# Optimization experiments

Hardware: AMD Instinct MI355X
Metric: run time of the kernel (lower is better)

## Reference

```python
import jax, jax.numpy as jnp
import numpy as np

V = 1024      # token vocab
C = 8         # n_codebooks
T = 256       # seg_len
BP = 4        # block_pairs (n_latent_blocks)
K = 512       # latent_vocab_size (codebook entries)
E = 128       # emb_dim
D = 128       # latent_dim / d_model
BETA = 0.05
NB = 6 * BP   # decoder sequence length = 24
NH = 4
HD = D // NH
FF = 512
R = 8
IN_FLAT = NB * D
OUT = T * C * V
B = 32


def setup_inputs() -> dict:
    key = jax.random.key(0)
    ks = jax.random.split(key, 20)
    n = lambda i, shape, s=0.02: jax.random.normal(ks[i], shape, jnp.float32) * s
    return {
        "tokens_prev": jax.random.randint(ks[0], (B, T, C), 0, V, jnp.int32),
        "tokens_curr": jax.random.randint(ks[1], (B, T, C), 0, V, jnp.int32),
        "tokens_next": jax.random.randint(ks[2], (B, T, C), 0, V, jnp.int32),
        "emb": n(3, (V, E)),
        "conv1_w": n(4, (4 * D, E * C, 3)),
        "conv1_b": jnp.zeros((4 * D,), jnp.float32),
        "conv2_w": n(5, (2 * D, 4 * D, 1)),
        "conv2_b": jnp.zeros((2 * D,), jnp.float32),
        "cb_instru": jax.random.uniform(ks[6], (K, D), jnp.float32, -1.0 / K, 1.0 / K),
        "cb_vocal": jax.random.uniform(ks[7], (K, D), jnp.float32, -1.0 / K, 1.0 / K),
        "pos": n(8, (1, NB, D), 1.0),
        "attn_in_w": n(9, (3 * D, D)),
        "attn_in_b": jnp.zeros((3 * D,), jnp.float32),
        "attn_out_w": n(10, (D, D)),
        "attn_out_b": jnp.zeros((D,), jnp.float32),
        "ln1_g": jnp.ones((D,), jnp.float32),
        "ln1_b": jnp.zeros((D,), jnp.float32),
        "lin1_w": n(11, (FF, D)),
        "lin1_b": jnp.zeros((FF,), jnp.float32),
        "lin2_w": n(12, (D, FF)),
        "lin2_b": jnp.zeros((D,), jnp.float32),
        "ln2_g": jnp.ones((D,), jnp.float32),
        "ln2_b": jnp.zeros((D,), jnp.float32),
        "lora_a": n(13, (R, IN_FLAT), 0.01),
        "lora_b": n(14, (OUT, R), 0.01),
    }


def _conv1d(x, w, b, pad):
    # x: (B, Cin, L), w: (Cout, Cin, Kw)
    y = jax.lax.conv_general_dilated(x, w, window_strides=(1,), padding=[(pad, pad)],
                                     dimension_numbers=("NCH", "OIH", "NCH"))
    return y + b[None, :, None]


def _encode(tokens, emb, w1, b1, w2, b2):
    Bb, Tt, Cc = tokens.shape
    x = emb[tokens].reshape(Bb, Tt, -1).transpose(0, 2, 1)       # (B, C*E, T)
    x = jax.nn.relu(_conv1d(x, w1, b1, 1))                        # (B, 4D, T)
    x = jax.nn.relu(_conv1d(x, w2, b2, 0))                        # (B, 2D, T)
    # AdaptiveAvgPool1d(BP) with T % BP == 0 -> mean over contiguous chunks
    x = x.reshape(Bb, 2 * D, BP, Tt // BP).mean(-1).transpose(0, 2, 1)  # (B, BP, 2D)
    return x[..., :D], x[..., D:]


def _vq(z, codebook):
    # z: (B, N, D); eval-mode VQ (no EMA update)
    Bb, N, Dd = z.shape
    flat = z.reshape(-1, Dd)
    dist = (jnp.sum(flat * flat, axis=1, keepdims=True)
            - 2.0 * flat @ codebook.T
            + jnp.sum(codebook * codebook, axis=1))
    codes = jnp.argmin(dist, axis=1)
    z_q = codebook[codes].reshape(Bb, N, Dd)
    commit = jnp.mean((z - jax.lax.stop_gradient(z_q)) ** 2)
    loss = BETA * commit
    z_q_st = z + jax.lax.stop_gradient(z_q - z)
    return z_q_st, codes.reshape(Bb, N), loss


def _layer_norm(x, g, b):
    mu = x.mean(-1, keepdims=True)
    var = ((x - mu) ** 2).mean(-1, keepdims=True)
    return (x - mu) * jax.lax.rsqrt(var + 1e-5) * g + b


def _tf_layer(x, in_w, in_b, out_w, out_b, g1, b1, w1, bb1, w2, bb2, g2, b2):
    # Post-norm TransformerEncoderLayer (relu, eval/no-dropout). x: (B, S, D)
    Bb, S, Dd = x.shape
    qkv = x @ in_w.T + in_b
    q, k, v = jnp.split(qkv, 3, axis=-1)
    q = q.reshape(Bb, S, NH, HD).transpose(0, 2, 1, 3)
    k = k.reshape(Bb, S, NH, HD).transpose(0, 2, 1, 3)
    v = v.reshape(Bb, S, NH, HD).transpose(0, 2, 1, 3)
    attn = jax.nn.softmax(jnp.einsum("bhsd,bhtd->bhst", q, k) / np.sqrt(HD), axis=-1)
    o = jnp.einsum("bhst,bhtd->bhsd", attn, v).transpose(0, 2, 1, 3).reshape(Bb, S, Dd)
    x = _layer_norm(x + o @ out_w.T + out_b, g1, b1)
    ff = jax.nn.relu(x @ w1.T + bb1) @ w2.T + bb2
    return _layer_norm(x + ff, g2, b2)


def reference(tokens_prev, tokens_curr, tokens_next, emb, conv1_w, conv1_b,
              conv2_w, conv2_b, cb_instru, cb_vocal, pos, attn_in_w, attn_in_b,
              attn_out_w, attn_out_b, ln1_g, ln1_b, lin1_w, lin1_b, lin2_w,
              lin2_b, ln2_g, ln2_b, lora_a, lora_b):
    p_i, p_v = _encode(tokens_prev, emb, conv1_w, conv1_b, conv2_w, conv2_b)
    c_i, c_v = _encode(tokens_curr, emb, conv1_w, conv1_b, conv2_w, conv2_b)
    n_i, n_v = _encode(tokens_next, emb, conv1_w, conv1_b, conv2_w, conv2_b)
    p_i_q, _, l1 = _vq(p_i, cb_instru)
    c_i_q, _, l2 = _vq(c_i, cb_instru)
    n_i_q, _, l3 = _vq(n_i, cb_instru)
    p_v_q, _, l4 = _vq(p_v, cb_vocal)
    c_v_q, _, l5 = _vq(c_v, cb_vocal)
    n_v_q, _, l6 = _vq(n_v, cb_vocal)
    vq_loss = l1 + l2 + l3 + l4 + l5 + l6
    z = jnp.concatenate([p_i_q, p_v_q, c_i_q, c_v_q, n_i_q, n_v_q], axis=1)  # (B, 24, D)
    z = z + pos[:, :z.shape[1], :]
    z = _tf_layer(z, attn_in_w, attn_in_b, attn_out_w, attn_out_b,
                  ln1_g, ln1_b, lin1_w, lin1_b, lin2_w, lin2_b, ln2_g, ln2_b)
    Bb = z.shape[0]
    flat = z.reshape(Bb, -1)
    logits = (flat @ lora_a.T) @ lora_b.T          # (B, T*C*V)
    logits = logits.reshape(Bb, T, C, V)
    logp = jax.nn.log_softmax(logits, axis=-1)
    nll = -jnp.take_along_axis(logp, tokens_curr[..., None].astype(jnp.int32), axis=-1)
    recon_loss = nll.mean()
    total_loss = recon_loss + vq_loss
    return total_loss
```

## Files before the change

kernel.cpp:

```cpp
#include <hip/hip_runtime.h>
#include <hip/hip_bf16.h>
#include <cstdint>
#include <cstddef>

typedef __attribute__((ext_vector_type(8))) short short8;
typedef __attribute__((ext_vector_type(4))) float floatx4;


__device__ __forceinline__ ushort f2bf(float f) {
    union { float f; unsigned int u; } x; x.f = f;
    unsigned int r = (x.u + 0x7fffu + ((x.u >> 16) & 1u)) >> 16;
    return (ushort)r;
}
__device__ __forceinline__ float bf2f(ushort u) {
    union { unsigned int u; float f; } x; x.u = ((unsigned int)u) << 16;
    return x.f;
}

__global__ __launch_bounds__(256) void prep_all(
    const float* __restrict__ emb, const float* __restrict__ w1,
    const float* __restrict__ w2, const float* __restrict__ cbi,
    const float* __restrict__ cbv, const float* __restrict__ aiw,
    const float* __restrict__ aow, const float* __restrict__ l1w,
    const float* __restrict__ l2w,
    ushort* __restrict__ ebf, ushort* __restrict__ w1bf, ushort* __restrict__ w2bf,
    float* __restrict__ cbiT, float* __restrict__ cbvT,
    ushort* __restrict__ aiwbf, ushort* __restrict__ aowbf,
    ushort* __restrict__ l1wbf, ushort* __restrict__ l2wbf,
    float* __restrict__ accum)
{
    int idx = blockIdx.x * 256 + threadIdx.x;
    if (idx < 4) accum[idx] = 0.f;
    if (idx < 131072) {
        ebf[idx] = f2bf(emb[idx]);
    } else if (idx < 262144) {
        int j = idx - 131072; w2bf[j] = f2bf(w2[j]);
    } else if (idx < 327680) {
        int j = idx - 262144; cbiT[(j & 127) * 512 + (j >> 7)] = cbi[j];
    } else if (idx < 393216) {
        int j = idx - 327680; cbvT[(j & 127) * 512 + (j >> 7)] = cbv[j];
    } else if (idx < 442368) {
        int j = idx - 393216; aiwbf[j] = f2bf(aiw[j]);
    } else if (idx < 475136) {
        int j = idx - 442368; aowbf[j] = f2bf(aow[j]);
    } else if (idx < 540672) {
        int j = idx - 475136; l1wbf[j] = f2bf(l1w[j]);
    } else if (idx < 606208) {
        int j = idx - 540672; l2wbf[j] = f2bf(l2w[j]);
    } else if (idx < 2179072) {
        int j = idx - 606208;
        int e  = j & 127;
        int co = (j >> 7) & 511;
        int cc = (j >> 16) & 7;
        int kw = j >> 19;
        w1bf[j] = f2bf(w1[(co * 1024 + cc * 128 + e) * 3 + kw]);
    }
}

__global__ __launch_bounds__(512, 4) void conv1_mfma(
    const int* __restrict__ tp, const int* __restrict__ tcu, const int* __restrict__ tn,
    const ushort* __restrict__ ebf, const ushort* __restrict__ w1bf,
    const float* __restrict__ b1, ushort* __restrict__ y1)
{
    constexpr int LDA = 136;
    __shared__ ushort As[130 * LDA];
    __shared__ ushort Bs[128 * LDA];
    __shared__ int tokL[130 * 8];
    const int tid = threadIdx.x;
    const int bx = blockIdx.x;
    const int nb = bx & 3, mb = bx >> 2;
    const int set = mb >> 6, rem = mb & 63, bb = rem >> 1, t0 = (rem & 1) << 7;
    const int n0 = nb << 7;
    const int* tok = (set == 0) ? tp : ((set == 1) ? tcu : tn);

    for (int idx = tid; idx < 1040; idx += 512) {
        const int row = idx >> 3, cc = idx & 7;
        const int gt = t0 + row - 1;
        tokL[idx] = (gt >= 0 && gt < 256) ? tok[bb * 2048 + gt * 8 + cc] : -1;
    }

    const int w = tid >> 6, lane = tid & 63;
    const int wm = w & 1, wn = w >> 1;
    const int rA = lane & 15, q4 = lane >> 4;
    const int ch = tid & 15, rowst = tid >> 4;

    floatx4 acc[4][2];
    for (int mi = 0; mi < 4; ++mi)
        for (int ni = 0; ni < 2; ++ni)
            acc[mi][ni] = (floatx4)(0.0f);

    __syncthreads();

    for (int cc = 0; cc < 8; ++cc) {
        for (int p = 0; p < 5; ++p) {
            const int row = p * 32 + rowst;
            if (row < 130) {
                const int tk = tokL[row * 8 + cc];
                uint4 val = make_uint4(0u, 0u, 0u, 0u);
                if (tk >= 0) val = *(const uint4*)(ebf + tk * 128 + ch * 8);
                *(uint4*)(As + row * LDA + ch * 8) = val;
            }
        }
        for (int kw = 0; kw < 3; ++kw) {
            const ushort* wsrc = w1bf + ((size_t)((kw * 8 + cc) * 512 + n0)) * 128;
            for (int p = 0; p < 4; ++p) {
                const int row = p * 32 + rowst;
                *(uint4*)(Bs + row * LDA + ch * 8) = *(const uint4*)(wsrc + row * 128 + ch * 8);
            }
            __syncthreads();
            for (int ks = 0; ks < 4; ++ks) {
                const int k0 = ks * 32 + q4 * 8;
                short8 a[4], bfr[2];
                for (int mi = 0; mi < 4; ++mi)
                    a[mi] = *(const short8*)(As + (wm * 64 + mi * 16 + rA + kw) * LDA + k0);
                for (int ni = 0; ni < 2; ++ni)
                    bfr[ni] = *(const short8*)(Bs + (wn * 32 + ni * 16 + rA) * LDA + k0);
                for (int mi = 0; mi < 4; ++mi)
                    for (int ni = 0; ni < 2; ++ni)
                        acc[mi][ni] = __builtin_amdgcn_mfma_f32_16x16x32_bf16(
                            a[mi], bfr[ni], acc[mi][ni], 0, 0, 0);
            }
            __syncthreads();
        }
    }
    for (int ni = 0; ni < 2; ++ni) {
        const int co = n0 + wn * 32 + ni * 16 + rA;
        const float bias = b1[co];
        for (int mi = 0; mi < 4; ++mi) {
            for (int r = 0; r < 4; ++r) {
                const int t = t0 + wm * 64 + mi * 16 + q4 * 4 + r;
                float v = acc[mi][ni][r] + bias;
                v = v > 0.f ? v : 0.f;
                y1[((size_t)(set * 32 + bb) * 256 + t) * 512 + co] = f2bf(v);
            }
        }
    }
}

__global__ __launch_bounds__(512, 4) void conv2_mfma(
    const ushort* __restrict__ y1, const ushort* __restrict__ w2bf,
    const float* __restrict__ b2, float* __restrict__ y2)
{
    constexpr int LDA = 136;
    __shared__ ushort As[128 * LDA];
    __shared__ ushort Bs[128 * LDA];
    __shared__ float pool[256];
    const int tid = threadIdx.x;
    const int bx = blockIdx.x;
    const int nb = bx & 1, mb = bx >> 1;
    const int set = mb >> 6, rem = mb & 63, bb = rem >> 1, t0 = (rem & 1) << 7;
    const int n0 = nb << 7;
    const int w = tid >> 6, lane = tid & 63;
    const int wm = w & 1, wn = w >> 1;
    const int rA = lane & 15, q4 = lane >> 4;
    const int ch = tid & 15, rowst = tid >> 4;

    floatx4 acc[4][2];
    for (int mi = 0; mi < 4; ++mi)
        for (int ni = 0; ni < 2; ++ni)
            acc[mi][ni] = (floatx4)(0.0f);

    const size_t arowbase = ((size_t)(set * 32 + bb) * 256 + t0) * 512;
    for (int kc = 0; kc < 4; ++kc) {
        for (int p = 0; p < 4; ++p) {
            const int row = p * 32 + rowst;
            *(uint4*)(As + row * LDA + ch * 8) =
                *(const uint4*)(y1 + arowbase + (size_t)row * 512 + kc * 128 + ch * 8);
            *(uint4*)(Bs + row * LDA + ch * 8) =
                *(const uint4*)(w2bf + (size_t)(n0 + row) * 512 + kc * 128 + ch * 8);
        }
        __syncthreads();
        for (int ks = 0; ks < 4; ++ks) {
            const int k0 = ks * 32 + q4 * 8;
            short8 a[4], bfr[2];
            for (int mi = 0; mi < 4; ++mi)
                a[mi] = *(const short8*)(As + (wm * 64 + mi * 16 + rA) * LDA + k0);
            for (int ni = 0; ni < 2; ++ni)
                bfr[ni] = *(const short8*)(Bs + (wn * 32 + ni * 16 + rA) * LDA + k0);
            for (int mi = 0; mi < 4; ++mi)
                for (int ni = 0; ni < 2; ++ni)
                    acc[mi][ni] = __builtin_amdgcn_mfma_f32_16x16x32_bf16(
                        a[mi], bfr[ni], acc[mi][ni], 0, 0, 0);
        }
        __syncthreads();
    }
    for (int ni = 0; ni < 2; ++ni) {
        const int col = wn * 32 + ni * 16 + rA;
        const float bias = b2[n0 + col];
        float s = 0.f;
        for (int mi = 0; mi < 4; ++mi)
            for (int r = 0; r < 4; ++r) {
                float v = acc[mi][ni][r] + bias;
                s += v > 0.f ? v : 0.f;
            }
        s += __shfl_xor(s, 16);
        s += __shfl_xor(s, 32);
        if (q4 == 0) pool[wm * 128 + col] = s;
    }
    __syncthreads();
    if (tid < 256) {
        const int wrow = tid >> 7, col = tid & 127;
        const int p = (t0 >> 6) + wrow;
        y2[((size_t)(set * 32 + bb) * 4 + p) * 256 + n0 + col] = pool[tid] * (1.f / 64.f);
    }
}

__global__ __launch_bounds__(256) void vq_kernel(
    const float* __restrict__ y2, const float* __restrict__ cbiT, const float* __restrict__ cbvT,
    const float* __restrict__ cbi, const float* __restrict__ cbv,
    const float* __restrict__ pos, float* __restrict__ ztr, ushort* __restrict__ xbf,
    float* __restrict__ accum)
{
    const int q = blockIdx.x;
    const int tid = threadIdx.x;
    const int set = q >> 7, bb = (q >> 2) & 31, p = q & 3;
    __shared__ float zloc[256];
    __shared__ float bestv[4];
    __shared__ int   besti[4];
    __shared__ int   code_sh[2];
    __shared__ float wsum2[4];
    zloc[tid] = y2[(size_t)q * 256 + tid];
    __syncthreads();
    const int w = tid >> 6, lane = tid & 63;
    const int half = w >> 1, sub = w & 1;
    const float4* cbT4 = (const float4*)(half ? cbvT : cbiT);
    const float* zh = zloc + half * 128;
    const int k4 = sub * 64 + lane;
    float a0 = 0.f, a1 = 0.f, a2 = 0.f, a3 = 0.f;
    for (int d = 0; d < 128; ++d) {
        float4 v = cbT4[d * 128 + k4];
        const float z = zh[d];
        float d0 = z - v.x, d1 = z - v.y, d2 = z - v.z, d3 = z - v.w;
        a0 += d0 * d0; a1 += d1 * d1; a2 += d2 * d2; a3 += d3 * d3;
    }
    float best = a0; int bidx = k4 * 4;
    if (a1 < best) { best = a1; bidx = k4 * 4 + 1; }
    if (a2 < best) { best = a2; bidx = k4 * 4 + 2; }
    if (a3 < best) { best = a3; bidx = k4 * 4 + 3; }
    for (int off = 32; off > 0; off >>= 1) {
        float ov = __shfl_xor(best, off);
        int   oi = __shfl_xor(bidx, off);
        if (ov < best || (ov == best && oi < bidx)) { best = ov; bidx = oi; }
    }
    if (lane == 0) { bestv[w] = best; besti[w] = bidx; }
    __syncthreads();
    if (tid < 2) {
        float v0 = bestv[tid * 2], v1 = bestv[tid * 2 + 1];
        int   i0 = besti[tid * 2], i1 = besti[tid * 2 + 1];
        code_sh[tid] = (v1 < v0 || (v1 == v0 && i1 < i0)) ? i1 : i0;
    }
    __syncthreads();
    const int hh = tid >> 7, d = tid & 127;
    const int code = code_sh[hh];
    const float* cb = hh ? cbv : cbi;
    const float zq = cb[code * 128 + d];
    const float diff = zloc[hh * 128 + d] - zq;
    float sq = diff * diff;
    for (int off = 32; off > 0; off >>= 1) sq += __shfl_xor(sq, off);
    if (lane == 0) wsum2[w] = sq;
    const int s = (set * 2 + hh) * 4 + p;
    const float val = zq + pos[s * 128 + d];
    ztr[((size_t)bb * 24 + s) * 128 + d] = val;
    xbf[((size_t)bb * 24 + s) * 128 + d] = f2bf(val);
    __syncthreads();
    if (tid == 0) atomicAdd(&accum[0], wsum2[0] + wsum2[1] + wsum2[2] + wsum2[3]);
}

template<int KTOT, int NTOT, int RELU, int OUTBF>
__global__ __launch_bounds__(256) void gemm64_kernel(
    const ushort* __restrict__ A, const ushort* __restrict__ Bw,
    const float* __restrict__ bias, void* __restrict__ Co)
{
    constexpr int NBLK = NTOT / 64;
    constexpr int LDA = 136;
    __shared__ ushort As[64 * LDA];
    __shared__ ushort Bs[64 * LDA];
    const int tid = threadIdx.x;
    const int mblk = blockIdx.x / NBLK, nblk = blockIdx.x % NBLK;
    const int m0 = mblk * 64, n0 = nblk * 64;
    const int w = tid >> 6, lane = tid & 63;
    const int rA = lane & 15, q4 = lane >> 4;
    const int ch = tid & 15, rowst = tid >> 4;

    floatx4 acc[4];
    for (int mi = 0; mi < 4; ++mi) acc[mi] = (floatx4)(0.f);

    for (int kc = 0; kc < KTOT / 128; ++kc) {
        for (int i = 0; i < 4; ++i) {
            const int row = i * 16 + rowst;
            *(uint4*)(As + row * LDA + ch * 8) =
                *(const uint4*)(A + (size_t)(m0 + row) * KTOT + kc * 128 + ch * 8);
            *(uint4*)(Bs + row * LDA + ch * 8) =
                *(const uint4*)(Bw + (size_t)(n0 + row) * KTOT + kc * 128 + ch * 8);
        }
        __syncthreads();
        for (int ks = 0; ks < 4; ++ks) {
            const int k0 = ks * 32 + q4 * 8;
            short8 bfr = *(const short8*)(Bs + (w * 16 + rA) * LDA + k0);
            for (int mi = 0; mi < 4; ++mi) {
                short8 a = *(const short8*)(As + (mi * 16 + rA) * LDA + k0);
                acc[mi] = __builtin_amdgcn_mfma_f32_16x16x32_bf16(a, bfr, acc[mi], 0, 0, 0);
            }
        }
        __syncthreads();
    }
    const int col = n0 + w * 16 + rA;
    const float bs = bias[col];
    for (int mi = 0; mi < 4; ++mi) {
        for (int r = 0; r < 4; ++r) {
            const int row = m0 + mi * 16 + q4 * 4 + r;
            float vv = acc[mi][r] + bs;
            if (RELU) vv = vv > 0.f ? vv : 0.f;
            if (OUTBF) ((ushort*)Co)[(size_t)row * NTOT + col] = f2bf(vv);
            else       ((float*)Co)[(size_t)row * NTOT + col]  = vv;
        }
    }
}

template<int KTOT, int WRITE_F32>
__global__ __launch_bounds__(256) void gemm_ln_kernel(
    const ushort* __restrict__ A, const ushort* __restrict__ Bw,
    const float* __restrict__ bias, const float* __restrict__ resid,
    const float* __restrict__ g, const float* __restrict__ beta,
    ushort* __restrict__ outbf, float* __restrict__ outf)
{
    constexpr int LDA = 136;
    __shared__ ushort As[64 * LDA];
    __shared__ ushort Bs[128 * LDA];
    __shared__ float ps[64 * 4], pq[64 * 4], muv[64], invv[64];
    const int tid = threadIdx.x;
    const int m0 = blockIdx.x * 64;
    const int w = tid >> 6, lane = tid & 63;
    const int rA = lane & 15, q4 = lane >> 4;
    const int ch = tid & 15, rowst = tid >> 4;

    floatx4 acc[4][2];
    for (int mi = 0; mi < 4; ++mi)
        for (int ni = 0; ni < 2; ++ni)
            acc[mi][ni] = (floatx4)(0.f);

    for (int kc = 0; kc < KTOT / 128; ++kc) {
        for (int i = 0; i < 4; ++i) {
            const int row = i * 16 + rowst;
            *(uint4*)(As + row * LDA + ch * 8) =
                *(const uint4*)(A + (size_t)(m0 + row) * KTOT + kc * 128 + ch * 8);
        }
        for (int i = 0; i < 8; ++i) {
            const int row = i * 16 + rowst;
            *(uint4*)(Bs + row * LDA + ch * 8) =
                *(const uint4*)(Bw + (size_t)row * KTOT + kc * 128 + ch * 8);
        }
        __syncthreads();
        for (int ks = 0; ks < 4; ++ks) {
            const int k0 = ks * 32 + q4 * 8;
            short8 a[4], bfr[2];
            for (int mi = 0; mi < 4; ++mi)
                a[mi] = *(const short8*)(As + (mi * 16 + rA) * LDA + k0);
            for (int ni = 0; ni < 2; ++ni)
                bfr[ni] = *(const short8*)(Bs + ((w * 2 + ni) * 16 + rA) * LDA + k0);
            for (int mi = 0; mi < 4; ++mi)
                for (int ni = 0; ni < 2; ++ni)
                    acc[mi][ni] = __builtin_amdgcn_mfma_f32_16x16x32_bf16(
                        a[mi], bfr[ni], acc[mi][ni], 0, 0, 0);
        }
        __syncthreads();
    }
    for (int ni = 0; ni < 2; ++ni) {
        const int col = (w * 2 + ni) * 16 + rA;
        const float bs = bias[col];
        for (int mi = 0; mi < 4; ++mi)
            for (int r = 0; r < 4; ++r) {
                const int row = m0 + mi * 16 + q4 * 4 + r;
                acc[mi][ni][r] += bs + resid[(size_t)row * 128 + col];
            }
    }
    for (int mi = 0; mi < 4; ++mi)
        for (int r = 0; r < 4; ++r) {
            float s  = acc[mi][0][r] + acc[mi][1][r];
            float sq = acc[mi][0][r] * acc[mi][0][r] + acc[mi][1][r] * acc[mi][1][r];
            for (int off = 1; off < 16; off <<= 1) {
                s  += __shfl_xor(s, off);
                sq += __shfl_xor(sq, off);
            }
            if (rA == 0) {
                const int rl = mi * 16 + q4 * 4 + r;
                ps[rl * 4 + w] = s;
                pq[rl * 4 + w] = sq;
            }
        }
    __syncthreads();
    if (tid < 64) {
        float s  = ps[tid * 4] + ps[tid * 4 + 1] + ps[tid * 4 + 2] + ps[tid * 4 + 3];
        float sq = pq[tid * 4] + pq[tid * 4 + 1] + pq[tid * 4 + 2] + pq[tid * 4 + 3];
        float mu = s * (1.f / 128.f);
        float var = sq * (1.f / 128.f) - mu * mu;
        muv[tid] = mu;
        invv[tid] = rsqrtf(var + 1e-5f);
    }
    __syncthreads();
    for (int ni = 0; ni < 2; ++ni) {
        const int col = (w * 2 + ni) * 16 + rA;
        const float gg = g[col], bb = beta[col];
        for (int mi = 0; mi < 4; ++mi)
            for (int r = 0; r < 4; ++r) {
                const int rl = mi * 16 + q4 * 4 + r;
                const int row = m0 + rl;
                float v = (acc[mi][ni][r] - muv[rl]) * invv[rl] * gg + bb;
                outbf[(size_t)row * 128 + col] = f2bf(v);
                if (WRITE_F32) outf[(size_t)row * 128 + col] = v;
            }
    }
}

__global__ __launch_bounds__(64) void attn_kernel(
    const float* __restrict__ qkvb, ushort* __restrict__ obuf)
{
    const int bh = blockIdx.x;
    const int b = bh >> 2, h = bh & 3;
    const int tid = threadIdx.x;
    __shared__ float q[24 * 32], k[24 * 32], v[24 * 32], sc[24 * 24];
    for (int i = 0; i < 12; ++i) {
        const int idx = i * 64 + tid;
        const int s = idx >> 5, d = idx & 31;
        const size_t base = ((size_t)(b * 24 + s)) * 384 + h * 32 + d;
        q[idx] = qkvb[base];
        k[idx] = qkvb[base + 128];
        v[idx] = qkvb[base + 256];
    }
    __syncthreads();
    for (int i = 0; i < 9; ++i) {
        const int e = i * 64 + tid;
        const int si = e / 24, j = e - si * 24;
        float a = 0.f;
        for (int d = 0; d < 32; ++d) a += q[si * 32 + d] * k[j * 32 + d];
        sc[si * 24 + j] = a * 0.17677669529663687f;
    }
    __syncthreads();
    if (tid < 24) {
        float* row = sc + tid * 24;
        float m = row[0];
        for (int j = 1; j < 24; ++j) m = row[j] > m ? row[j] : m;
        float ssum = 0.f;
        for (int j = 0; j < 24; ++j) { float e = __expf(row[j] - m); row[j] = e; ssum += e; }
        float inv = 1.f / ssum;
        for (int j = 0; j < 24; ++j) row[j] *= inv;
    }
    __syncthreads();
    for (int i = 0; i < 12; ++i) {
        const int idx = i * 64 + tid;
        const int s = idx >> 5, d = idx & 31;
        float a = 0.f;
        for (int j = 0; j < 24; ++j) a += sc[s * 24 + j] * v[j * 32 + d];
        obuf[((size_t)(b * 24 + s)) * 128 + h * 32 + d] = f2bf(a);
    }
}

__global__ __launch_bounds__(256) void lora_kernel(
    const ushort* __restrict__ zbf, const float* __restrict__ lora_a,
    float* __restrict__ hbuf)
{
    const int b = blockIdx.x;
    const int tid = threadIdx.x;
    const int w = tid >> 6, lane = tid & 63;
    __shared__ float zl[3072];
    for (int idx = tid; idx < 3072; idx += 256) zl[idx] = bf2f(zbf[(size_t)b * 3072 + idx]);
    __syncthreads();
    for (int rr = 0; rr < 2; ++rr) {
        const int r = w + rr * 4;
        float acc = 0.f;
        for (int idx = lane; idx < 3072; idx += 64)
            acc += lora_a[(size_t)r * 3072 + idx] * zl[idx];
        for (int off = 32; off > 0; off >>= 1) acc += __shfl_xor(acc, off);
        if (lane == 0) hbuf[b * 8 + r] = acc;
    }
}

__global__ __launch_bounds__(256) void logits_kernel(
    const float* __restrict__ hbuf, const float* __restrict__ lora_b,
    const int* __restrict__ tokc, float* __restrict__ accum, float* __restrict__ out)
{
    const int tid = threadIdx.x;
    const int tcb = blockIdx.x;
    __shared__ float hl[256];
    __shared__ float wsum[4];
    __shared__ float ltok;
    hl[tid] = hbuf[tid];
    float wr[4][8];
    for (int i = 0; i < 4; ++i) {
        const float4* pw = (const float4*)(lora_b + ((size_t)tcb * 1024 + tid + 256 * i) * 8);
        float4 x = pw[0], y = pw[1];
        wr[i][0] = x.x; wr[i][1] = x.y; wr[i][2] = x.z; wr[i][3] = x.w;
        wr[i][4] = y.x; wr[i][5] = y.y; wr[i][6] = y.z; wr[i][7] = y.w;
    }
    __syncthreads();
    float nll = 0.f;
    for (int bb = 0; bb < 32; ++bb) {
        const int tv = tokc[bb * 2048 + tcb];
        const float* h = hl + bb * 8;
        float h0 = h[0], h1 = h[1], h2 = h[2], h3 = h[3];
        float h4 = h[4], h5 = h[5], h6 = h[6], h7 = h[7];
        float sl = 0.f;
        for (int i = 0; i < 4; ++i) {
            float lg = h0 * wr[i][0] + h1 * wr[i][1] + h2 * wr[i][2] + h3 * wr[i][3]
                     + h4 * wr[i][4] + h5 * wr[i][5] + h6 * wr[i][6] + h7 * wr[i][7];
            sl += __expf(lg);
            if (tid + 256 * i == tv) ltok = lg;
        }
        for (int off = 32; off > 0; off >>= 1) sl += __shfl_xor(sl, off);
        if ((tid & 63) == 0) wsum[tid >> 6] = sl;
        __syncthreads();
        if (tid == 0) nll += logf(wsum[0] + wsum[1] + wsum[2] + wsum[3]) - ltok;
        __syncthreads();
    }
    if (tid == 0) {
        atomicAdd(&accum[1], nll);
        __threadfence();
        unsigned int prev = atomicAdd((unsigned int*)(accum + 2), 1u);
        if (prev == 2047u) {
            float vq  = atomicAdd(&accum[0], 0.f);
            float rec = atomicAdd(&accum[1], 0.f);
            out[0] = rec * (1.f / 65536.f) + 0.05f * vq * (1.f / 16384.f);
        }
    }
}

extern "C" void kernel_launch(void* const* d_in, const int* in_sizes, int n_in,
                              void* d_out, int out_size, void* d_ws, size_t ws_size,
                              hipStream_t stream) {
    const int*   tp   = (const int*)d_in[0];
    const int*   tcu  = (const int*)d_in[1];
    const int*   tn   = (const int*)d_in[2];
    const float* emb  = (const float*)d_in[3];
    const float* w1   = (const float*)d_in[4];
    const float* b1   = (const float*)d_in[5];
    const float* w2   = (const float*)d_in[6];
    const float* b2   = (const float*)d_in[7];
    const float* cbi  = (const float*)d_in[8];
    const float* cbv  = (const float*)d_in[9];
    const float* pos  = (const float*)d_in[10];
    const float* aiw  = (const float*)d_in[11];
    const float* aib  = (const float*)d_in[12];
    const float* aow  = (const float*)d_in[13];
    const float* aob  = (const float*)d_in[14];
    const float* g1   = (const float*)d_in[15];
    const float* be1  = (const float*)d_in[16];
    const float* l1w  = (const float*)d_in[17];
    const float* l1b  = (const float*)d_in[18];
    const float* l2w  = (const float*)d_in[19];
    const float* l2b  = (const float*)d_in[20];
    const float* g2   = (const float*)d_in[21];
    const float* be2  = (const float*)d_in[22];
    const float* lra  = (const float*)d_in[23];
    const float* lrb  = (const float*)d_in[24];

    char* wsb = (char*)d_ws;
    ushort* ebf  = (ushort*)(wsb + 0);
    ushort* w1bf = (ushort*)(wsb + 262144);
    ushort* w2bf = (ushort*)(wsb + 3407872);
    float*  cbiT = (float*)(wsb + 3670016);
    float*  cbvT = (float*)(wsb + 3932160);
    ushort* y1   = (ushort*)(wsb + 4194304);
    float*  y2   = (float*)(wsb + 29360128);
    float*  ztr  = (float*)(wsb + 29753344);
    float*  hbuf = (float*)(wsb + 30146560);
    float*  accum= (float*)(wsb + 30147584);
    ushort* aiwbf= (ushort*)(wsb + 30147648);
    ushort* aowbf= (ushort*)(wsb + 30245952);
    ushort* l1wbf= (ushort*)(wsb + 30278720);
    ushort* l2wbf= (ushort*)(wsb + 30409792);
    if (ws_size < 30540864) return;

    float*  qkvb = (float*)(wsb + 4194304);
    ushort* obuf = (ushort*)(wsb + 5373952);
    ushort* x1bf = (ushort*)(wsb + 5570560);
    float*  x1f  = (float*)(wsb + 5767168);
    ushort* hff  = (ushort*)(wsb + 6160384);
    ushort* zbf  = (ushort*)(wsb + 6946816);
    ushort* xbf  = (ushort*)(wsb + 7143424);

    prep_all<<<8512, 256, 0, stream>>>(emb, w1, w2, cbi, cbv, aiw, aow, l1w, l2w,
                                       ebf, w1bf, w2bf, cbiT, cbvT,
                                       aiwbf, aowbf, l1wbf, l2wbf, accum);
    conv1_mfma<<<768, 512, 0, stream>>>(tp, tcu, tn, ebf, w1bf, b1, y1);
    conv2_mfma<<<384, 512, 0, stream>>>(y1, w2bf, b2, y2);
    vq_kernel<<<384, 256, 0, stream>>>(y2, cbiT, cbvT, cbi, cbv, pos, ztr, xbf, accum);
    gemm64_kernel<128, 384, 0, 0><<<72, 256, 0, stream>>>(xbf, aiwbf, aib, qkvb);
    attn_kernel<<<128, 64, 0, stream>>>(qkvb, obuf);
    gemm_ln_kernel<128, 1><<<12, 256, 0, stream>>>(obuf, aowbf, aob, ztr, g1, be1, x1bf, x1f);
    gemm64_kernel<128, 512, 1, 1><<<96, 256, 0, stream>>>(x1bf, l1wbf, l1b, hff);
    gemm_ln_kernel<512, 0><<<12, 256, 0, stream>>>(hff, l2wbf, l2b, x1f, g2, be2, zbf, nullptr);
    lora_kernel<<<32, 256, 0, stream>>>(zbf, lra, hbuf);
    logits_kernel<<<2048, 256, 0, stream>>>(hbuf, lrb, tcu, accum, (float*)d_out);
}
```

Baseline: 404.4 us.

## Precompute embedding-conv1 product table and fuse transformer tail into persistent kernel

```diff
diff --git a/kernel.cpp b/kernel.cpp
--- a/kernel.cpp
+++ b/kernel.cpp
@@ -15,6 +15,17 @@
 __device__ __forceinline__ float bf2f(ushort u) {
     union { unsigned int u; float f; } x; x.u = ((unsigned int)u) << 16;
     return x.f;
+}
+
+__device__ __forceinline__ void gbar(unsigned int* bar, unsigned int nb) {
+    __threadfence();
+    __syncthreads();
+    if (threadIdx.x == 0) {
+        atomicAdd(bar, 1u);
+        while (atomicAdd(bar, 0u) < nb) __builtin_amdgcn_s_sleep(2);
+    }
+    __syncthreads();
+    __threadfence();
 }
 
 __global__ __launch_bounds__(256) void prep_all(
@@ -30,7 +41,7 @@
     float* __restrict__ accum)
 {
     int idx = blockIdx.x * 256 + threadIdx.x;
-    if (idx < 4) accum[idx] = 0.f;
+    if (idx < 16) accum[idx] = 0.f;
     if (idx < 131072) {
         ebf[idx] = f2bf(emb[idx]);
     } else if (idx < 262144) {
@@ -57,6 +68,108 @@
     }
 }
 
+__global__ __launch_bounds__(512) void ubuild_kernel(
+    const ushort* __restrict__ ebf, const ushort* __restrict__ w1bf,
+    ushort* __restrict__ U)
+{
+    constexpr int LDA = 136;
+    __shared__ ushort As[128 * LDA];
+    __shared__ ushort Bs[128 * LDA];
+    const int tid = threadIdx.x;
+    const int bx = blockIdx.x;
+    const int kc = bx >> 5, rem = bx & 31, mt = rem >> 2, nt = rem & 3;
+    const int v0 = mt << 7, co0 = nt << 7;
+    const int w = tid >> 6, lane = tid & 63;
+    const int wm = w & 1, wn = w >> 1;
+    const int rA = lane & 15, q4 = lane >> 4;
+    const int ch = tid & 15, rowst = tid >> 4;
+
+    for (int p = 0; p < 4; ++p) {
+        const int row = p * 32 + rowst;
+        *(uint4*)(As + row * LDA + ch * 8) =
+            *(const uint4*)(ebf + (size_t)(v0 + row) * 128 + ch * 8);
+        *(uint4*)(Bs + row * LDA + ch * 8) =
+            *(const uint4*)(w1bf + (size_t)kc * 65536 + (size_t)(co0 + row) * 128 + ch * 8);
+    }
+    __syncthreads();
+
+    floatx4 acc[4][2];
+    for (int mi = 0; mi < 4; ++mi)
+        for (int ni = 0; ni < 2; ++ni)
+            acc[mi][ni] = (floatx4)(0.0f);
+    for (int ks = 0; ks < 4; ++ks) {
+        const int k0 = ks * 32 + q4 * 8;
+        short8 a[4], bfr[2];
+        for (int mi = 0; mi < 4; ++mi)
+            a[mi] = *(const short8*)(As + (wm * 64 + mi * 16 + rA) * LDA + k0);
+        for (int ni = 0; ni < 2; ++ni)
+            bfr[ni] = *(const short8*)(Bs + (wn * 32 + ni * 16 + rA) * LDA + k0);
+        for (int mi = 0; mi < 4; ++mi)
+            for (int ni = 0; ni < 2; ++ni)
+                acc[mi][ni] = __builtin_amdgcn_mfma_f32_16x16x32_bf16(
+                    a[mi], bfr[ni], acc[mi][ni], 0, 0, 0);
+    }
+    for (int ni = 0; ni < 2; ++ni) {
+        const int col = co0 + wn * 32 + ni * 16 + rA;
+        for (int mi = 0; mi < 4; ++mi)
+            for (int r = 0; r < 4; ++r) {
+                const int row = v0 + wm * 64 + mi * 16 + q4 * 4 + r;
+                U[((size_t)kc * 1024 + row) * 512 + col] = f2bf(acc[mi][ni][r]);
+            }
+    }
+}
+
+__global__ __launch_bounds__(256) void conv1_gather(
+    const int* __restrict__ tp, const int* __restrict__ tcu, const int* __restrict__ tn,
+    const ushort* __restrict__ U, const float* __restrict__ b1,
+    ushort* __restrict__ y1)
+{
+    __shared__ int tokL[34 * 8];
+    const int bx = blockIdx.x;
+    const int set = bx >> 8, bb = (bx >> 3) & 31, pp = bx & 7;
+    const int t0 = pp << 5;
+    const int* tok = (set == 0) ? tp : ((set == 1) ? tcu : tn);
+    const int tid = threadIdx.x;
+    const int w = tid >> 6, lane = tid & 63;
+
+    for (int idx = tid; idx < 272; idx += 256) {
+        const int row = idx >> 3, cc = idx & 7;
+        const int gt = t0 + row - 1;
+        tokL[idx] = (gt >= 0 && gt < 256) ? tok[bb * 2048 + gt * 8 + cc] : -1;
+    }
+    float bias[8];
+    {
+        const float4* b4 = (const float4*)(b1 + lane * 8);
+        float4 x = b4[0], y = b4[1];
+        bias[0] = x.x; bias[1] = x.y; bias[2] = x.z; bias[3] = x.w;
+        bias[4] = y.x; bias[5] = y.y; bias[6] = y.z; bias[7] = y.w;
+    }
+    __syncthreads();
+
+    const size_t outbase = ((size_t)(set * 32 + bb) * 256 + t0) * 512 + lane * 8;
+    for (int tl = 0; tl < 8; ++tl) {
+        const int row = w * 8 + tl;
+        float acc[8];
+        for (int j = 0; j < 8; ++j) acc[j] = bias[j];
+        for (int kw = 0; kw < 3; ++kw) {
+            const int* trow = tokL + (row + kw) * 8;
+            for (int cc = 0; cc < 8; ++cc) {
+                const int u = trow[cc];
+                if (u >= 0) {
+                    const short8 s = *(const short8*)(U + (((size_t)(kw * 8 + cc) * 1024 + u) * 512 + lane * 8));
+                    for (int j = 0; j < 8; ++j) acc[j] += bf2f((ushort)s[j]);
+                }
+            }
+        }
+        ushort o[8];
+        for (int j = 0; j < 8; ++j) {
+            float v = acc[j];
+            o[j] = f2bf(v > 0.f ? v : 0.f);
+        }
+        *(uint4*)(y1 + outbase + (size_t)row * 512) = *(const uint4*)o;
+    }
+}
+
 __global__ __launch_bounds__(512, 4) void conv1_mfma(
     const int* __restrict__ tp, const int* __restrict__ tcu, const int* __restrict__ tn,
     const ushort* __restrict__ ebf, const ushort* __restrict__ w1bf,
@@ -266,39 +379,33 @@
     if (tid == 0) atomicAdd(&accum[0], wsum2[0] + wsum2[1] + wsum2[2] + wsum2[3]);
 }
 
-template<int KTOT, int NTOT, int RELU, int OUTBF>
-__global__ __launch_bounds__(256) void gemm64_kernel(
-    const ushort* __restrict__ A, const ushort* __restrict__ Bw,
-    const float* __restrict__ bias, void* __restrict__ Co)
-{
-    constexpr int NBLK = NTOT / 64;
-    constexpr int LDA = 136;
-    __shared__ ushort As[64 * LDA];
-    __shared__ ushort Bs[64 * LDA];
-    const int tid = threadIdx.x;
-    const int mblk = blockIdx.x / NBLK, nblk = blockIdx.x % NBLK;
+__device__ void gemm64_dev(const ushort* __restrict__ A, const ushort* __restrict__ Bw,
+                           const float* __restrict__ bias, float* Cof, ushort* Cobf,
+                           int KTOT, int NTOT, bool relu, int mblk, int nblk, char* SMEM)
+{
+    ushort* As = (ushort*)SMEM;
+    ushort* Bs = (ushort*)(SMEM + 17408);
+    const int tid = threadIdx.x;
     const int m0 = mblk * 64, n0 = nblk * 64;
     const int w = tid >> 6, lane = tid & 63;
     const int rA = lane & 15, q4 = lane >> 4;
     const int ch = tid & 15, rowst = tid >> 4;
-
     floatx4 acc[4];
     for (int mi = 0; mi < 4; ++mi) acc[mi] = (floatx4)(0.f);
-
     for (int kc = 0; kc < KTOT / 128; ++kc) {
         for (int i = 0; i < 4; ++i) {
             const int row = i * 16 + rowst;
-            *(uint4*)(As + row * LDA + ch * 8) =
+            *(uint4*)(As + row * 136 + ch * 8) =
                 *(const uint4*)(A + (size_t)(m0 + row) * KTOT + kc * 128 + ch * 8);
-            *(uint4*)(Bs + row * LDA + ch * 8) =
+            *(uint4*)(Bs + row * 136 + ch * 8) =
                 *(const uint4*)(Bw + (size_t)(n0 + row) * KTOT + kc * 128 + ch * 8);
         }
         __syncthreads();
         for (int ks = 0; ks < 4; ++ks) {
             const int k0 = ks * 32 + q4 * 8;
-            short8 bfr = *(const short8*)(Bs + (w * 16 + rA) * LDA + k0);
+            short8 bfr = *(const short8*)(Bs + (w * 16 + rA) * 136 + k0);
             for (int mi = 0; mi < 4; ++mi) {
-                short8 a = *(const short8*)(As + (mi * 16 + rA) * LDA + k0);
+                short8 a = *(const short8*)(As + (mi * 16 + rA) * 136 + k0);
                 acc[mi] = __builtin_amdgcn_mfma_f32_16x16x32_bf16(a, bfr, acc[mi], 0, 0, 0);
             }
         }
@@ -306,30 +413,29 @@
     }
     const int col = n0 + w * 16 + rA;
     const float bs = bias[col];
-    for (int mi = 0; mi < 4; ++mi) {
+    for (int mi = 0; mi < 4; ++mi)
         for (int r = 0; r < 4; ++r) {
             const int row = m0 + mi * 16 + q4 * 4 + r;
             float vv = acc[mi][r] + bs;
-            if (RELU) vv = vv > 0.f ? vv : 0.f;
-            if (OUTBF) ((ushort*)Co)[(size_t)row * NTOT + col] = f2bf(vv);
-            else       ((float*)Co)[(size_t)row * NTOT + col]  = vv;
-        }
-    }
-}
-
-template<int KTOT, int WRITE_F32>
-__global__ __launch_bounds__(256) void gemm_ln_kernel(
-    const ushort* __restrict__ A, const ushort* __restrict__ Bw,
-    const float* __restrict__ bias, const float* __restrict__ resid,
-    const float* __restrict__ g, const float* __restrict__ beta,
-    ushort* __restrict__ outbf, float* __restrict__ outf)
-{
-    constexpr int LDA = 136;
-    __shared__ ushort As[64 * LDA];
-    __shared__ ushort Bs[128 * LDA];
-    __shared__ float ps[64 * 4], pq[64 * 4], muv[64], invv[64];
-    const int tid = threadIdx.x;
-    const int m0 = blockIdx.x * 64;
+            if (relu) vv = vv > 0.f ? vv : 0.f;
+            if (Cobf) Cobf[(size_t)row * NTOT + col] = f2bf(vv);
+            else      Cof[(size_t)row * NTOT + col]  = vv;
+        }
+}
+
+__device__ void gemm_ln_dev(const ushort* __restrict__ A, const ushort* __restrict__ Bw,
+                            const float* __restrict__ bias, const float* __restrict__ resid,
+                            const float* __restrict__ g, const float* __restrict__ beta,
+                            ushort* outbf, float* outf, int KTOT, int mblk, char* SMEM)
+{
+    ushort* As  = (ushort*)SMEM;
+    ushort* Bs  = (ushort*)(SMEM + 17408);
+    float*  ps  = (float*)(SMEM + 52224);
+    float*  pq  = (float*)(SMEM + 53248);
+    float*  muv = (float*)(SMEM + 54272);
+    float*  inv = (float*)(SMEM + 54528);
+    const int tid = threadIdx.x;
+    const int m0 = mblk * 64;
     const int w = tid >> 6, lane = tid & 63;
     const int rA = lane & 15, q4 = lane >> 4;
     const int ch = tid & 15, rowst = tid >> 4;
@@ -342,12 +448,12 @@
     for (int kc = 0; kc < KTOT / 128; ++kc) {
         for (int i = 0; i < 4; ++i) {
             const int row = i * 16 + rowst;
-            *(uint4*)(As + row * LDA + ch * 8) =
+            *(uint4*)(As + row * 136 + ch * 8) =
                 *(const uint4*)(A + (size_t)(m0 + row) * KTOT + kc * 128 + ch * 8);
         }
         for (int i = 0; i < 8; ++i) {
             const int row = i * 16 + rowst;
-            *(uint4*)(Bs + row * LDA + ch * 8) =
+            *(uint4*)(Bs + row * 136 + ch * 8) =
                 *(const uint4*)(Bw + (size_t)row * KTOT + kc * 128 + ch * 8);
         }
         __syncthreads();
@@ -355,9 +461,9 @@
             const int k0 = ks * 32 + q4 * 8;
             short8 a[4], bfr[2];
             for (int mi = 0; mi < 4; ++mi)
-                a[mi] = *(const short8*)(As + (mi * 16 + rA) * LDA + k0);
+                a[mi] = *(const short8*)(As + (mi * 16 + rA) * 136 + k0);
             for (int ni = 0; ni < 2; ++ni)
-                bfr[ni] = *(const short8*)(Bs + ((w * 2 + ni) * 16 + rA) * LDA + k0);
+                bfr[ni] = *(const short8*)(Bs + ((w * 2 + ni) * 16 + rA) * 136 + k0);
             for (int mi = 0; mi < 4; ++mi)
                 for (int ni = 0; ni < 2; ++ni)
                     acc[mi][ni] = __builtin_amdgcn_mfma_f32_16x16x32_bf16(
@@ -395,7 +501,7 @@
         float mu = s * (1.f / 128.f);
         float var = sq * (1.f / 128.f) - mu * mu;
         muv[tid] = mu;
-        invv[tid] = rsqrtf(var + 1e-5f);
+        inv[tid] = rsqrtf(var + 1e-5f);
     }
     __syncthreads();
     for (int ni = 0; ni < 2; ++ni) {
@@ -405,73 +511,99 @@
             for (int r = 0; r < 4; ++r) {
                 const int rl = mi * 16 + q4 * 4 + r;
                 const int row = m0 + rl;
-                float v = (acc[mi][ni][r] - muv[rl]) * invv[rl] * gg + bb;
-                outbf[(size_t)row * 128 + col] = f2bf(v);
-                if (WRITE_F32) outf[(size_t)row * 128 + col] = v;
-            }
-    }
-}
-
-__global__ __launch_bounds__(64) void attn_kernel(
-    const float* __restrict__ qkvb, ushort* __restrict__ obuf)
-{
-    const int bh = blockIdx.x;
-    const int b = bh >> 2, h = bh & 3;
-    const int tid = threadIdx.x;
-    __shared__ float q[24 * 32], k[24 * 32], v[24 * 32], sc[24 * 24];
-    for (int i = 0; i < 12; ++i) {
-        const int idx = i * 64 + tid;
-        const int s = idx >> 5, d = idx & 31;
-        const size_t base = ((size_t)(b * 24 + s)) * 384 + h * 32 + d;
-        q[idx] = qkvb[base];
-        k[idx] = qkvb[base + 128];
-        v[idx] = qkvb[base + 256];
-    }
-    __syncthreads();
-    for (int i = 0; i < 9; ++i) {
-        const int e = i * 64 + tid;
-        const int si = e / 24, j = e - si * 24;
-        float a = 0.f;
-        for (int d = 0; d < 32; ++d) a += q[si * 32 + d] * k[j * 32 + d];
-        sc[si * 24 + j] = a * 0.17677669529663687f;
-    }
-    __syncthreads();
-    if (tid < 24) {
-        float* row = sc + tid * 24;
-        float m = row[0];
-        for (int j = 1; j < 24; ++j) m = row[j] > m ? row[j] : m;
-        float ssum = 0.f;
-        for (int j = 0; j < 24; ++j) { float e = __expf(row[j] - m); row[j] = e; ssum += e; }
-        float inv = 1.f / ssum;
-        for (int j = 0; j < 24; ++j) row[j] *= inv;
-    }
-    __syncthreads();
-    for (int i = 0; i < 12; ++i) {
-        const int idx = i * 64 + tid;
-        const int s = idx >> 5, d = idx & 31;
-        float a = 0.f;
-        for (int j = 0; j < 24; ++j) a += sc[s * 24 + j] * v[j * 32 + d];
-        obuf[((size_t)(b * 24 + s)) * 128 + h * 32 + d] = f2bf(a);
-    }
-}
-
-__global__ __launch_bounds__(256) void lora_kernel(
-    const ushort* __restrict__ zbf, const float* __restrict__ lora_a,
-    float* __restrict__ hbuf)
-{
-    const int b = blockIdx.x;
-    const int tid = threadIdx.x;
-    const int w = tid >> 6, lane = tid & 63;
-    __shared__ float zl[3072];
-    for (int idx = tid; idx < 3072; idx += 256) zl[idx] = bf2f(zbf[(size_t)b * 3072 + idx]);
-    __syncthreads();
-    for (int rr = 0; rr < 2; ++rr) {
-        const int r = w + rr * 4;
-        float acc = 0.f;
-        for (int idx = lane; idx < 3072; idx += 64)
-            acc += lora_a[(size_t)r * 3072 + idx] * zl[idx];
-        for (int off = 32; off > 0; off >>= 1) acc += __shfl_xor(acc, off);
-        if (lane == 0) hbuf[b * 8 + r] = acc;
+                float v = (acc[mi][ni][r] - muv[rl]) * inv[rl] * gg + bb;
+                if (outbf) outbf[(size_t)row * 128 + col] = f2bf(v);
+                if (outf)  outf[(size_t)row * 128 + col]  = v;
+            }
+    }
+}
+
+__global__ __launch_bounds__(256) void tail_pk(
+    const ushort* __restrict__ xbf, const float* __restrict__ ztr,
+    const ushort* __restrict__ aiwbf, const float* __restrict__ aib,
+    const ushort* __restrict__ aowbf, const float* __restrict__ aob,
+    const float* __restrict__ g1, const float* __restrict__ be1,
+    const ushort* __restrict__ l1wbf, const float* __restrict__ l1b,
+    const ushort* __restrict__ l2wbf, const float* __restrict__ l2b,
+    const float* __restrict__ g2, const float* __restrict__ be2,
+    const float* __restrict__ lora_a,
+    float* __restrict__ QKV, ushort* __restrict__ obuf,
+    ushort* __restrict__ x1bf, float* __restrict__ x1f,
+    ushort* __restrict__ hff, float* __restrict__ zf,
+    float* __restrict__ hbuf, unsigned int* __restrict__ bar)
+{
+    __shared__ __align__(16) char SM[55296];
+    const unsigned int NB = 96;
+    const int bx = blockIdx.x;
+    const int tid = threadIdx.x;
+
+    if (bx < 72) gemm64_dev(xbf, aiwbf, aib, QKV, nullptr, 128, 384, false, bx / 6, bx % 6, SM);
+    gbar(bar + 0, NB);
+
+    if (bx < 32) {
+        const int b = bx;
+        const int w = tid >> 6, lane = tid & 63;
+        float* F = (float*)SM + w * 2880;
+        float* q = F; float* k = F + 768; float* v = F + 1536; float* sc = F + 2304;
+        for (int l = 0; l < 12; ++l) {
+            const int idx = l * 64 + lane;
+            const int s = idx >> 5, d = idx & 31;
+            const size_t base = ((size_t)(b * 24 + s)) * 384 + w * 32 + d;
+            q[idx] = QKV[base];
+            k[idx] = QKV[base + 128];
+            v[idx] = QKV[base + 256];
+        }
+        __syncthreads();
+        for (int l = 0; l < 9; ++l) {
+            const int e = l * 64 + lane;
+            const int i = e / 24, j = e - i * 24;
+            float s = 0.f;
+            for (int d = 0; d < 32; ++d) s += q[i * 32 + d] * k[j * 32 + d];
+            sc[i * 24 + j] = s * 0.17677669529663687f;
+        }
+        __syncthreads();
+        if (lane < 24) {
+            float* row = sc + lane * 24;
+            float m = row[0];
+            for (int j = 1; j < 24; ++j) m = row[j] > m ? row[j] : m;
+            float ssum = 0.f;
+            for (int j = 0; j < 24; ++j) { float e = __expf(row[j] - m); row[j] = e; ssum += e; }
+            float iv = 1.f / ssum;
+            for (int j = 0; j < 24; ++j) row[j] *= iv;
+        }
+        __syncthreads();
+        for (int l = 0; l < 12; ++l) {
+            const int idx = l * 64 + lane;
+            const int s = idx >> 5, d = idx & 31;
+            float a = 0.f;
+            for (int j = 0; j < 24; ++j) a += sc[s * 24 + j] * v[j * 32 + d];
+            obuf[((size_t)(b * 24 + s)) * 128 + w * 32 + d] = f2bf(a);
+        }
+    }
+    gbar(bar + 1, NB);
+
+    if (bx < 12) gemm_ln_dev(obuf, aowbf, aob, ztr, g1, be1, x1bf, x1f, 128, bx, SM);
+    gbar(bar + 2, NB);
+
+    if (bx < 96) gemm64_dev(x1bf, l1wbf, l1b, nullptr, hff, 128, 512, true, bx / 8, bx % 8, SM);
+    gbar(bar + 3, NB);
+
+    if (bx < 12) gemm_ln_dev(hff, l2wbf, l2b, x1f, g2, be2, nullptr, zf, 512, bx, SM);
+    gbar(bar + 4, NB);
+
+    if (bx < 32) {
+        float* zl = (float*)SM;
+        for (int i = tid; i < 3072; i += 256) zl[i] = zf[(size_t)bx * 3072 + i];
+        __syncthreads();
+        const int w = tid >> 6, lane = tid & 63;
+        for (int rr = 0; rr < 2; ++rr) {
+            const int r = w + rr * 4;
+            float a = 0.f;
+            for (int i = lane; i < 3072; i += 64)
+                a += lora_a[(size_t)r * 3072 + i] * zl[i];
+            for (int off = 32; off > 0; off >>= 1) a += __shfl_xor(a, off);
+            if (lane == 0) hbuf[bx * 8 + r] = a;
+        }
     }
 }
 
@@ -568,27 +700,32 @@
     ushort* aowbf= (ushort*)(wsb + 30245952);
     ushort* l1wbf= (ushort*)(wsb + 30278720);
     ushort* l2wbf= (ushort*)(wsb + 30409792);
+    ushort* U    = (ushort*)(wsb + 30541824);
     if (ws_size < 30540864) return;
-
-    float*  qkvb = (float*)(wsb + 4194304);
+    const bool use_u = (ws_size >= 55707648);
+
+    float*  QKV  = (float*)(wsb + 4194304);
     ushort* obuf = (ushort*)(wsb + 5373952);
     ushort* x1bf = (ushort*)(wsb + 5570560);
     float*  x1f  = (float*)(wsb + 5767168);
     ushort* hff  = (ushort*)(wsb + 6160384);
-    ushort* zbf  = (ushort*)(wsb + 6946816);
-    ushort* xbf  = (ushort*)(wsb + 7143424);
+    float*  zf   = (float*)(wsb + 6946816);
+    ushort* xbf  = (ushort*)(wsb + 7340032);
 
     prep_all<<<8512, 256, 0, stream>>>(emb, w1, w2, cbi, cbv, aiw, aow, l1w, l2w,
                                        ebf, w1bf, w2bf, cbiT, cbvT,
                                        aiwbf, aowbf, l1wbf, l2wbf, accum);
-    conv1_mfma<<<768, 512, 0, stream>>>(tp, tcu, tn, ebf, w1bf, b1, y1);
+    if (use_u) {
+        ubuild_kernel<<<768, 512, 0, stream>>>(ebf, w1bf, U);
+        conv1_gather<<<768, 256, 0, stream>>>(tp, tcu, tn, U, b1, y1);
+    } else {
+        conv1_mfma<<<768, 512, 0, stream>>>(tp, tcu, tn, ebf, w1bf, b1, y1);
+    }
     conv2_mfma<<<384, 512, 0, stream>>>(y1, w2bf, b2, y2);
     vq_kernel<<<384, 256, 0, stream>>>(y2, cbiT, cbvT, cbi, cbv, pos, ztr, xbf, accum);
-    gemm64_kernel<128, 384, 0, 0><<<72, 256, 0, stream>>>(xbf, aiwbf, aib, qkvb);
-    attn_kernel<<<128, 64, 0, stream>>>(qkvb, obuf);
-    gemm_ln_kernel<128, 1><<<12, 256, 0, stream>>>(obuf, aowbf, aob, ztr, g1, be1, x1bf, x1f);
-    gemm64_kernel<128, 512, 1, 1><<<96, 256, 0, stream>>>(x1bf, l1wbf, l1b, hff);
-    gemm_ln_kernel<512, 0><<<12, 256, 0, stream>>>(hff, l2wbf, l2b, x1f, g2, be2, zbf, nullptr);
-    lora_kernel<<<32, 256, 0, stream>>>(zbf, lra, hbuf);
+    tail_pk<<<96, 256, 0, stream>>>(xbf, ztr, aiwbf, aib, aowbf, aob, g1, be1,
+                                    l1wbf, l1b, l2wbf, l2b, g2, be2, lra,
+                                    QKV, obuf, x1bf, x1f, hff, zf, hbuf,
+                                    (unsigned int*)(accum + 4));
     logits_kernel<<<2048, 256, 0, stream>>>(hbuf, lrb, tcu, accum, (float*)d_out);
 }
```

New measurement: 484.9 us. 19.9% more time.
